# Kernel optimization log

Hardware: AMD Instinct MI355X
Metric: run time of the kernel (lower is better)

Reference implementation:

```python
import jax, jax.numpy as jnp
import numpy as np

B, S, D_MODEL, D_K = 4, 4096, 1024, 64


def setup_inputs() -> dict:
    key = jax.random.key(0)
    ks = jax.random.split(key, 4)
    scale = 1.0 / np.sqrt(D_MODEL)
    x = jax.random.normal(ks[0], (B, S, D_MODEL), dtype=jnp.float32)
    Wq = jax.random.normal(ks[1], (D_MODEL, D_K), dtype=jnp.float32) * scale
    Wk = jax.random.normal(ks[2], (D_MODEL, D_K), dtype=jnp.float32) * scale
    Wv = jax.random.normal(ks[3], (D_MODEL, D_K), dtype=jnp.float32) * scale
    bq = jnp.zeros((D_K,), dtype=jnp.float32)
    bk = jnp.zeros((D_K,), dtype=jnp.float32)
    bv = jnp.zeros((D_K,), dtype=jnp.float32)
    # causal mask: 1 = keep, 0 = masked (matches docstring semantics)
    mask = jnp.broadcast_to(
        jnp.tril(jnp.ones((S, S), dtype=jnp.int32))[None], (B, S, S)
    )
    return {"x": x, "mask": mask, "Wq": Wq, "bq": bq, "Wk": Wk, "bk": bk, "Wv": Wv, "bv": bv}


def reference(x, mask, Wq, bq, Wk, bk, Wv, bv):
    # Q/K/V projections: (B, S, d_model) @ (d_model, d_k) -> (B, S, d_k)
    Q = jnp.einsum("bsd,dk->bsk", x, Wq) + bq
    K = jnp.einsum("bsd,dk->bsk", x, Wk) + bk
    V = jnp.einsum("bsd,dk->bsk", x, Wv) + bv
    # scaled dot-product scores: (B, S, S)
    scores = jnp.einsum("bqk,bsk->bqs", Q, K) / jnp.sqrt(jnp.float32(D_K))
    scores = jnp.where(mask == 0, jnp.float32(-jnp.inf), scores)
    attn = jax.nn.softmax(scores, axis=-1)
    # dropout with p_drop = 0.0 is identity
    out = jnp.einsum("bqs,bsk->bqk", attn, V)  # (B, S, d_k)
    return out
```

## Files before the change

### kernel.cpp

```cpp
#include <hip/hip_runtime.h>
#include <hip/hip_bf16.h>


typedef float  f32x4 __attribute__((ext_vector_type(4)));
typedef short  s16x8 __attribute__((ext_vector_type(8)));
typedef short  s16x4 __attribute__((ext_vector_type(4)));

#define MFMA16(A, B, C) __builtin_amdgcn_mfma_f32_16x16x32_bf16((A), (B), (C), 0, 0, 0)

static __device__ __forceinline__ ushort f2bf(float f) {
    union { float f; unsigned u; } v; v.f = f;
    unsigned u = v.u;
    unsigned r = (u + 0x7FFFu + ((u >> 16) & 1u)) >> 16;
    return (ushort)r;
}

static __device__ __forceinline__ f32x4 fzero() {
    f32x4 v; v[0] = v[1] = v[2] = v[3] = 0.f; return v;
}

__global__ __launch_bounds__(256) void prep_w(const float* __restrict__ Wq,
                                              const float* __restrict__ Wk,
                                              const float* __restrict__ Wv,
                                              short* __restrict__ Wt) {
    const int c = blockIdx.x;
    const int t = threadIdx.x;
    const float* src; int cc; float sc = 1.0f;
    if (c < 64)       { src = Wq; cc = c;       sc = 0.125f; }
    else if (c < 128) { src = Wk; cc = c - 64;  }
    else              { src = Wv; cc = c - 128; }
    const int k0 = t * 4;
    s16x4 o;
    #pragma unroll
    for (int i = 0; i < 4; ++i) o[i] = (short)f2bf(src[(size_t)(k0 + i) * 64 + cc] * sc);
    *(s16x4*)&Wt[(size_t)c * 1024 + k0] = o;
}

__global__ __launch_bounds__(128) void proj(const float* __restrict__ x,
                                            const short* __restrict__ Wt,
                                            const float* __restrict__ bq,
                                            const float* __restrict__ bk,
                                            const float* __restrict__ bv,
                                            short* __restrict__ Qb,
                                            short* __restrict__ Kb,
                                            short* __restrict__ Vt) {
    const int tid  = threadIdx.x;
    const int lane = tid & 63;
    const int w    = tid >> 6;
    const int m0   = blockIdx.x * 32;
    const int l15  = lane & 15, gr = lane >> 4;

    f32x4 acc[6][2];
    #pragma unroll
    for (int m = 0; m < 6; ++m)
        for (int n = 0; n < 2; ++n) acc[m][n] = fzero();

    const short* aptr = Wt + (size_t)(96 * w + l15) * 1024 + 8 * gr;
    const float* bptr = x  + (size_t)(m0 + l15) * 1024 + 8 * gr;

    for (int kt = 0; kt < 32; ++kt) {
        const int ko = kt * 32;
        s16x8 a[6];
        #pragma unroll
        for (int m = 0; m < 6; ++m) a[m] = *(const s16x8*)(aptr + (size_t)m * 16 * 1024 + ko);
        #pragma unroll
        for (int n = 0; n < 2; ++n) {
            f32x4 b0 = *(const f32x4*)(bptr + (size_t)n * 16 * 1024 + ko);
            f32x4 b1 = *(const f32x4*)(bptr + (size_t)n * 16 * 1024 + ko + 4);
            s16x8 bb;
            bb[0] = (short)f2bf(b0[0]); bb[1] = (short)f2bf(b0[1]);
            bb[2] = (short)f2bf(b0[2]); bb[3] = (short)f2bf(b0[3]);
            bb[4] = (short)f2bf(b1[0]); bb[5] = (short)f2bf(b1[1]);
            bb[6] = (short)f2bf(b1[2]); bb[7] = (short)f2bf(b1[3]);
            #pragma unroll
            for (int m = 0; m < 6; ++m) acc[m][n] = MFMA16(a[m], bb, acc[m][n]);
        }
    }

    #pragma unroll
    for (int m = 0; m < 6; ++m) {
        const int c0 = 96 * w + 16 * m + 4 * gr;
        #pragma unroll
        for (int n = 0; n < 2; ++n) {
            const int row = m0 + 16 * n + l15;
            f32x4 v = acc[m][n];
            if (c0 < 64) {
                s16x4 o;
                #pragma unroll
                for (int r = 0; r < 4; ++r) o[r] = (short)f2bf(v[r] + 0.125f * bq[c0 + r]);
                *(s16x4*)&Qb[(size_t)row * 64 + c0] = o;
            } else if (c0 < 128) {
                s16x4 o;
                #pragma unroll
                for (int r = 0; r < 4; ++r) o[r] = (short)f2bf(v[r] + bk[c0 - 64 + r]);
                *(s16x4*)&Kb[(size_t)row * 64 + (c0 - 64)] = o;
            } else {
                const int b = row >> 12, s = row & 4095;
                #pragma unroll
                for (int r = 0; r < 4; ++r)
                    Vt[((size_t)b * 64 + (c0 - 128 + r)) * 4096 + s] =
                        (short)f2bf(v[r] + bv[c0 - 128 + r]);
            }
        }
    }
}

__global__ __launch_bounds__(256) void attn(const short* __restrict__ Qb,
                                            const short* __restrict__ Kb,
                                            const short* __restrict__ Vt,
                                            float* __restrict__ out) {
    const int bid   = blockIdx.x;
    const int batch = bid & 3;
    const int g     = 127 - (bid >> 2);
    const int q0    = g * 32;
    const int tid   = threadIdx.x, lane = tid & 63, w = tid >> 6;
    const int l15   = lane & 15, gr = lane >> 4;

    __shared__ short P_lds[4][32][72];
    __shared__ float Om[4][32][64];
    __shared__ float Mm[4][32], Lm[4][32];

    const size_t qrow0 = (size_t)batch * 4096;

    s16x8 qf[2][2];
    #pragma unroll
    for (int ms = 0; ms < 2; ++ms)
        for (int f = 0; f < 2; ++f)
            qf[ms][f] = *(const s16x8*)&Qb[(qrow0 + q0 + 16 * ms + l15) * 64 + 32 * f + 8 * gr];

    f32x4 o[2][4];
    float mreg[2][4], lreg[2][4];
    #pragma unroll
    for (int ms = 0; ms < 2; ++ms) {
        for (int n = 0; n < 4; ++n) o[ms][n] = fzero();
        for (int r = 0; r < 4; ++r) { mreg[ms][r] = -1e30f; lreg[ms][r] = 0.f; }
    }

    const int L  = q0 + 32;
    const int nt = (L + 63) >> 6;
    const int t0 = (nt * w) >> 2, t1 = (nt * (w + 1)) >> 2;

    const short* Kbase = Kb + qrow0 * 64;
    const short* Vbase = Vt + (size_t)batch * 64 * 4096;

    for (int t = t0; t < t1; ++t) {
        const int j0 = t << 6;
        s16x8 kf[4][2], vf[4][2];
        #pragma unroll
        for (int n = 0; n < 4; ++n)
            for (int f = 0; f < 2; ++f) {
                kf[n][f] = *(const s16x8*)&Kbase[(size_t)(j0 + 16 * n + l15) * 64 + 32 * f + 8 * gr];
                vf[n][f] = *(const s16x8*)&Vbase[(size_t)(16 * n + l15) * 4096 + j0 + 32 * f + 8 * gr];
            }

        const bool needmask = (j0 + 63 > q0);
        #pragma unroll
        for (int ms = 0; ms < 2; ++ms) {
            f32x4 s[4];
            #pragma unroll
            for (int n = 0; n < 4; ++n) {
                s[n] = fzero();
                for (int f = 0; f < 2; ++f) s[n] = MFMA16(qf[ms][f], kf[n][f], s[n]);
            }
            if (needmask) {
                const int qrow = q0 + 16 * ms + 4 * gr;
                #pragma unroll
                for (int n = 0; n < 4; ++n) {
                    const int j = j0 + 16 * n + l15;
                    for (int r = 0; r < 4; ++r)
                        if (j > qrow + r) s[n][r] = -1e30f;
                }
            }
            float tm[4];
            #pragma unroll
            for (int r = 0; r < 4; ++r)
                tm[r] = fmaxf(fmaxf(s[0][r], s[1][r]), fmaxf(s[2][r], s[3][r]));
            #pragma unroll
            for (int d = 1; d < 16; d <<= 1)
                for (int r = 0; r < 4; ++r) tm[r] = fmaxf(tm[r], __shfl_xor(tm[r], d));

            float p[4][4];
            #pragma unroll
            for (int r = 0; r < 4; ++r) {
                const float mn = fmaxf(mreg[ms][r], tm[r]);
                const float sc = __expf(mreg[ms][r] - mn);
                mreg[ms][r] = mn;
                lreg[ms][r] *= sc;
                for (int n = 0; n < 4; ++n) o[ms][n][r] *= sc;
                float ls = 0.f;
                for (int n = 0; n < 4; ++n) { float e = __expf(s[n][r] - mn); p[n][r] = e; ls += e; }
                lreg[ms][r] += ls;
            }
            #pragma unroll
            for (int n = 0; n < 4; ++n)
                for (int r = 0; r < 4; ++r)
                    P_lds[w][16 * ms + 4 * gr + r][16 * n + l15] = (short)f2bf(p[n][r]);
        }
        #pragma unroll
        for (int ms = 0; ms < 2; ++ms) {
            s16x8 pf[2];
            for (int f = 0; f < 2; ++f)
                pf[f] = *(const s16x8*)&P_lds[w][16 * ms + l15][32 * f + 8 * gr];
            #pragma unroll
            for (int n = 0; n < 4; ++n)
                for (int f = 0; f < 2; ++f)
                    o[ms][n] = MFMA16(pf[f], vf[n][f], o[ms][n]);
        }
    }

    #pragma unroll
    for (int ms = 0; ms < 2; ++ms)
        for (int d = 1; d < 16; d <<= 1)
            for (int r = 0; r < 4; ++r) lreg[ms][r] += __shfl_xor(lreg[ms][r], d);

    #pragma unroll
    for (int ms = 0; ms < 2; ++ms) {
        for (int n = 0; n < 4; ++n)
            for (int r = 0; r < 4; ++r)
                Om[w][16 * ms + 4 * gr + r][16 * n + l15] = o[ms][n][r];
        if (l15 == 0)
            for (int r = 0; r < 4; ++r) {
                Mm[w][16 * ms + 4 * gr + r] = mreg[ms][r];
                Lm[w][16 * ms + 4 * gr + r] = lreg[ms][r];
            }
    }
    __syncthreads();

    {
        const int r  = tid >> 3;
        const int d0 = (tid & 7) * 8;
        const float mt = fmaxf(fmaxf(Mm[0][r], Mm[1][r]), fmaxf(Mm[2][r], Mm[3][r]));
        float lt = 0.f;
        f32x4 a0 = fzero(), a1 = fzero();
        #pragma unroll
        for (int ww = 0; ww < 4; ++ww) {
            const float sc = __expf(Mm[ww][r] - mt);
            lt += sc * Lm[ww][r];
            f32x4 v0 = *(const f32x4*)&Om[ww][r][d0];
            f32x4 v1 = *(const f32x4*)&Om[ww][r][d0 + 4];
            #pragma unroll
            for (int j = 0; j < 4; ++j) { a0[j] += sc * v0[j]; a1[j] += sc * v1[j]; }
        }
        const float inv = 1.f / lt;
        const size_t ob = (qrow0 + q0 + r) * 64 + d0;
        f32x4 r0, r1;
        #pragma unroll
        for (int j = 0; j < 4; ++j) { r0[j] = a0[j] * inv; r1[j] = a1[j] * inv; }
        *(f32x4*)&out[ob]     = r0;
        *(f32x4*)&out[ob + 4] = r1;
    }
}

extern "C" void kernel_launch(void* const* d_in, const int* in_sizes, int n_in,
                              void* d_out, int out_size, void* d_ws, size_t ws_size,
                              hipStream_t stream) {
    const float* x  = (const float*)d_in[0];
    const float* Wq = (const float*)d_in[2];
    const float* bq = (const float*)d_in[3];
    const float* Wk = (const float*)d_in[4];
    const float* bk = (const float*)d_in[5];
    const float* Wv = (const float*)d_in[6];
    const float* bv = (const float*)d_in[7];
    float* out = (float*)d_out;

    char* ws = (char*)d_ws;
    short* Wt = (short*)(ws);
    short* Qb = (short*)(ws + 393216);
    short* Kb = (short*)(ws + 2490368);
    short* Vt = (short*)(ws + 4587520);

    prep_w<<<dim3(192), dim3(256), 0, stream>>>(Wq, Wk, Wv, Wt);
    proj<<<dim3(512), dim3(128), 0, stream>>>(x, Wt, bq, bk, bv, Qb, Kb, Vt);
    attn<<<dim3(512), dim3(256), 0, stream>>>(Qb, Kb, Vt, out);
}
```

Baseline: 99.75 us.

## Stage x tiles in double-buffered LDS shared across four waves in projection

The projection kernel now has four waves per block cooperatively load x from global memory, convert it to bf16 once, and store it in a padded double-buffered shared-memory tile. Each wave then reads its MFMA B operand from LDS and computes a narrower 48-column slice. This removes the redundant per-wave global loads and bf16 conversions of the activation tile and overlaps the next chunk's global load with compute. In exchange it adds LDS traffic and a barrier per chunk.

```diff
diff --git a/kernel.cpp b/kernel.cpp
--- a/kernel.cpp
+++ b/kernel.cpp
@@ -36,7 +36,7 @@
     *(s16x4*)&Wt[(size_t)c * 1024 + k0] = o;
 }
 
-__global__ __launch_bounds__(128) void proj(const float* __restrict__ x,
+__global__ __launch_bounds__(256) void proj(const float* __restrict__ x,
                                             const short* __restrict__ Wt,
                                             const float* __restrict__ bq,
                                             const float* __restrict__ bk,
@@ -50,36 +50,65 @@
     const int m0   = blockIdx.x * 32;
     const int l15  = lane & 15, gr = lane >> 4;
 
-    f32x4 acc[6][2];
-    #pragma unroll
-    for (int m = 0; m < 6; ++m)
+    __shared__ short xs[2][32][136];
+
+    const int srow = tid >> 3;
+    const int sc8  = tid & 7;
+    const float* sbase = x + (size_t)(m0 + srow) * 1024 + 4 * sc8;
+
+    f32x4 acc[3][2];
+    #pragma unroll
+    for (int m = 0; m < 3; ++m)
         for (int n = 0; n < 2; ++n) acc[m][n] = fzero();
 
-    const short* aptr = Wt + (size_t)(96 * w + l15) * 1024 + 8 * gr;
-    const float* bptr = x  + (size_t)(m0 + l15) * 1024 + 8 * gr;
-
-    for (int kt = 0; kt < 32; ++kt) {
-        const int ko = kt * 32;
-        s16x8 a[6];
-        #pragma unroll
-        for (int m = 0; m < 6; ++m) a[m] = *(const s16x8*)(aptr + (size_t)m * 16 * 1024 + ko);
-        #pragma unroll
-        for (int n = 0; n < 2; ++n) {
-            f32x4 b0 = *(const f32x4*)(bptr + (size_t)n * 16 * 1024 + ko);
-            f32x4 b1 = *(const f32x4*)(bptr + (size_t)n * 16 * 1024 + ko + 4);
-            s16x8 bb;
-            bb[0] = (short)f2bf(b0[0]); bb[1] = (short)f2bf(b0[1]);
-            bb[2] = (short)f2bf(b0[2]); bb[3] = (short)f2bf(b0[3]);
-            bb[4] = (short)f2bf(b1[0]); bb[5] = (short)f2bf(b1[1]);
-            bb[6] = (short)f2bf(b1[2]); bb[7] = (short)f2bf(b1[3]);
-            #pragma unroll
-            for (int m = 0; m < 6; ++m) acc[m][n] = MFMA16(a[m], bb, acc[m][n]);
-        }
-    }
-
-    #pragma unroll
-    for (int m = 0; m < 6; ++m) {
-        const int c0 = 96 * w + 16 * m + 4 * gr;
+    const short* aptr = Wt + (size_t)(48 * w + l15) * 1024 + 8 * gr;
+
+    f32x4 ld[4];
+    #pragma unroll
+    for (int i = 0; i < 4; ++i) ld[i] = *(const f32x4*)(sbase + 32 * i);
+    #pragma unroll
+    for (int i = 0; i < 4; ++i) {
+        s16x4 o;
+        #pragma unroll
+        for (int j = 0; j < 4; ++j) o[j] = (short)f2bf(ld[i][j]);
+        *(s16x4*)&xs[0][srow][4 * sc8 + 32 * i] = o;
+    }
+    __syncthreads();
+
+    for (int c = 0; c < 8; ++c) {
+        const int buf = c & 1;
+        if (c < 7) {
+            #pragma unroll
+            for (int i = 0; i < 4; ++i) ld[i] = *(const f32x4*)(sbase + 128 * (c + 1) + 32 * i);
+        }
+        #pragma unroll
+        for (int f = 0; f < 4; ++f) {
+            const int ko = 128 * c + 32 * f;
+            s16x8 a[3];
+            #pragma unroll
+            for (int m = 0; m < 3; ++m) a[m] = *(const s16x8*)(aptr + (size_t)m * 16 * 1024 + ko);
+            s16x8 b[2];
+            #pragma unroll
+            for (int n = 0; n < 2; ++n) b[n] = *(const s16x8*)&xs[buf][16 * n + l15][32 * f + 8 * gr];
+            #pragma unroll
+            for (int m = 0; m < 3; ++m)
+                for (int n = 0; n < 2; ++n) acc[m][n] = MFMA16(a[m], b[n], acc[m][n]);
+        }
+        if (c < 7) {
+            #pragma unroll
+            for (int i = 0; i < 4; ++i) {
+                s16x4 o;
+                #pragma unroll
+                for (int j = 0; j < 4; ++j) o[j] = (short)f2bf(ld[i][j]);
+                *(s16x4*)&xs[buf ^ 1][srow][4 * sc8 + 32 * i] = o;
+            }
+        }
+        __syncthreads();
+    }
+
+    #pragma unroll
+    for (int m = 0; m < 3; ++m) {
+        const int c0 = 48 * w + 16 * m + 4 * gr;
         #pragma unroll
         for (int n = 0; n < 2; ++n) {
             const int row = m0 + 16 * n + l15;
@@ -270,6 +299,6 @@
     short* Vt = (short*)(ws + 4587520);
 
     prep_w<<<dim3(192), dim3(256), 0, stream>>>(Wq, Wk, Wv, Wt);
-    proj<<<dim3(512), dim3(128), 0, stream>>>(x, Wt, bq, bk, bv, Qb, Kb, Vt);
+    proj<<<dim3(512), dim3(256), 0, stream>>>(x, Wt, bq, bk, bv, Qb, Kb, Vt);
     attn<<<dim3(512), dim3(256), 0, stream>>>(Qb, Kb, Vt, out);
 }
```

Measured after the change: 91.18 us. 8.6% less time.
